# Optimization experiments

Hardware: AMD Instinct MI355X
Metric: run time of the kernel (lower is better)

## Reference

```python
import jax, jax.numpy as jnp
import numpy as np

NQ = 10          # num_qubits
NL = 4           # num_layers (StronglyEntanglingLayers)
DIM = 2 ** NQ    # state-vector dimension = input_linear out features
B = 4096
SEQ = 512
PRED = 96

# ---- static basis-state bookkeeping (wire 0 = most significant bit, as in PennyLane) ----

def _cnot_perm(control, target):
    s = np.arange(DIM)
    bit = (s >> (NQ - 1 - control)) & 1
    return s ^ (bit << (NQ - 1 - target))

def _layer_perms():
    # StronglyEntanglingLayers default ranges: r_l = (l % (n_wires - 1)) + 1,
    # then CNOT(i, (i+r) % n) for i = 0..n-1, applied sequentially.
    perms = []
    for l in range(NL):
        r = (l % (NQ - 1)) + 1
        comp = np.arange(DIM)
        for c in range(NQ):
            g = _cnot_perm(c, (c + r) % NQ)
            comp = comp[g]          # compose: state_new[t] = state_old[comp[t]]
        perms.append(jnp.asarray(comp))
    return perms

PERMS = _layer_perms()

_bits = (np.arange(DIM)[:, None] >> (NQ - 1 - np.arange(NQ))[None, :]) & 1
SIGNS = jnp.asarray(1.0 - 2.0 * _bits, dtype=np.float32)   # [DIM, NQ] PauliZ eigenvalues


def _rot_gates(w):
    # PennyLane Rot(phi, theta, omega) = RZ(omega) @ RY(theta) @ RZ(phi); w: [L, n, 3]
    phi, theta, omega = w[..., 0], w[..., 1], w[..., 2]
    c = jnp.cos(theta / 2)
    s = jnp.sin(theta / 2)
    ep = jnp.exp(0.5j * (phi + omega))   # e^{+i(phi+omega)/2}
    em = jnp.exp(0.5j * (phi - omega))   # e^{+i(phi-omega)/2}
    m00 = jnp.conj(ep) * c
    m01 = -em * s
    m10 = jnp.conj(em) * s
    m11 = ep * c
    return jnp.stack([jnp.stack([m00, m01], -1),
                      jnp.stack([m10, m11], -1)], -2)       # [L, n, 2, 2] complex64


def _apply_1q(psi, U, wire):
    # psi: [B, DIM] complex; apply 2x2 U on `wire`
    b = psi.shape[0]
    left = 2 ** wire
    right = 2 ** (NQ - 1 - wire)
    psi = psi.reshape(b, left, 2, right)
    psi = jnp.einsum('ba,kpaq->kpbq', U, psi)
    return psi.reshape(b, DIM)


def _circuit(psi, q_weights):
    mats = _rot_gates(q_weights)
    for l in range(NL):
        for w in range(NQ):
            psi = _apply_1q(psi, mats[l, w], w)
        psi = psi[:, PERMS[l]]          # composed CNOT ring of this layer
    return psi


def reference(x, W_in, b_in, q_weights, W_out, b_out):
    h = x @ W_in.T + b_in + 1e-6                          # input_linear, then +1e-6
    norm = jnp.linalg.norm(h, axis=-1, keepdims=True)
    psi = (h / norm).astype(jnp.complex64)                # AmplitudeEmbedding(normalize=True)
    psi = _circuit(psi, q_weights)                        # StronglyEntanglingLayers
    probs = psi.real ** 2 + psi.imag ** 2
    expvals = probs @ SIGNS                               # [B, NQ] PauliZ expvals
    return expvals @ W_out.T + b_out                      # output_linear


def setup_inputs() -> dict:
    key = jax.random.key(0)
    ks = jax.random.split(key, 6)
    x = jax.random.normal(ks[0], (B, SEQ), dtype=jnp.float32)
    W_in = jax.random.normal(ks[1], (DIM, SEQ), dtype=jnp.float32) / np.sqrt(SEQ)
    b_in = jax.random.normal(ks[2], (DIM,), dtype=jnp.float32) * 0.01
    q_weights = jax.random.uniform(ks[3], (NL, NQ, 3), dtype=jnp.float32,
                                   minval=0.0, maxval=2.0 * np.pi)
    W_out = jax.random.normal(ks[4], (PRED, NQ), dtype=jnp.float32) / np.sqrt(NQ)
    b_out = jax.random.normal(ks[5], (PRED,), dtype=jnp.float32) * 0.01
    return {"x": x, "W_in": W_in, "b_in": b_in, "q_weights": q_weights,
            "W_out": W_out, "b_out": b_out}
```

## Files before the change

kernel.cpp:

```cpp
#include <hip/hip_runtime.h>
#include <math.h>

#define DIM 1024
#define NQ 10
#define NL 4
#define SEQ 512
#define NROWS 4096
#define PRED 96

typedef unsigned short ushort_t;
typedef unsigned int uint_t;
using half8   = __attribute__((ext_vector_type(8))) _Float16;
using float4v = __attribute__((ext_vector_type(4))) float;

__device__ inline ushort_t f2h(float f) { _Float16 h = (_Float16)f; return *(ushort_t*)&h; }
__device__ inline uint_t pkh(float a, float b) {
    _Float16 ha = (_Float16)a, hb = (_Float16)b;
    return (uint_t)(*(ushort_t*)&ha) | ((uint_t)(*(ushort_t*)&hb) << 16);
}

__global__ __launch_bounds__(256)
void convert_x_kernel(const float* __restrict__ x, ushort_t* __restrict__ xh)
{
    int i = (blockIdx.x * 256 + threadIdx.x) * 8;
    float4 a = *(const float4*)(x + i);
    float4 b = *(const float4*)(x + i + 4);
    uint4 o;
    o.x = pkh(a.x, a.y); o.y = pkh(a.z, a.w);
    o.z = pkh(b.x, b.y); o.w = pkh(b.z, b.w);
    *(uint4*)(xh + i) = o;
}

__global__ __launch_bounds__(512)
void circuit_cols_kernel(const float* __restrict__ Wi, const float* __restrict__ b_in,
                         const float* __restrict__ qw,
                         ushort_t* __restrict__ Crt_r, ushort_t* __restrict__ Crt_i,
                         float* __restrict__ dr, float* __restrict__ di)
{
    __shared__ float2 psi[DIM];
    __shared__ float gm[NL * NQ][8];

    const int tid = threadIdx.x;
    const int j = blockIdx.x;

    if (tid < NL * NQ) {
        float phi = qw[tid * 3 + 0], theta = qw[tid * 3 + 1], omega = qw[tid * 3 + 2];
        float ch = cosf(theta * 0.5f), sh = sinf(theta * 0.5f);
        float a = 0.5f * (phi + omega), b = 0.5f * (phi - omega);
        float ca = cosf(a), sa = sinf(a);
        float cb = cosf(b), sb = sinf(b);
        gm[tid][0] =  ch * ca;  gm[tid][1] = -ch * sa;
        gm[tid][2] = -sh * cb;  gm[tid][3] = -sh * sb;
        gm[tid][4] =  sh * cb;  gm[tid][5] = -sh * sb;
        gm[tid][6] =  ch * ca;  gm[tid][7] =  ch * sa;
    }

    float v0, v1;
    if (j < SEQ) {
        v0 = Wi[(size_t)(2 * tid) * SEQ + j];
        v1 = Wi[(size_t)(2 * tid + 1) * SEQ + j];
    } else {
        v0 = b_in[2 * tid] + 1e-6f;
        v1 = b_in[2 * tid + 1] + 1e-6f;
    }
    psi[2 * tid]     = make_float2(v0, 0.f);
    psi[2 * tid + 1] = make_float2(v1, 0.f);
    __syncthreads();

    for (int l = 0; l < NL; ++l) {
#pragma unroll
        for (int w = 0; w < NQ; ++w) {
            const float* m = gm[l * NQ + w];
            float m00r = m[0], m00i = m[1], m01r = m[2], m01i = m[3];
            float m10r = m[4], m10i = m[5], m11r = m[6], m11i = m[7];
            int mask = 1 << (9 - w);
            int lo = tid & (mask - 1);
            int s0 = ((tid ^ lo) << 1) | lo;
            int s1 = s0 | mask;
            float2 a0 = psi[s0], a1 = psi[s1];
            float2 n0, n1;
            n0.x = m00r * a0.x - m00i * a0.y + m01r * a1.x - m01i * a1.y;
            n0.y = m00r * a0.y + m00i * a0.x + m01r * a1.y + m01i * a1.x;
            n1.x = m10r * a0.x - m10i * a0.y + m11r * a1.x - m11i * a1.y;
            n1.y = m10r * a0.y + m10i * a0.x + m11r * a1.y + m11i * a1.x;
            psi[s0] = n0; psi[s1] = n1;
            __syncthreads();
        }
        int r = l % (NQ - 1) + 1;
        int p0 = tid, p1 = tid + 512;
#pragma unroll
        for (int c = 9; c >= 0; --c) {
            int t = (c + r) % NQ;
            p0 ^= ((p0 >> (9 - c)) & 1) << (9 - t);
            p1 ^= ((p1 >> (9 - c)) & 1) << (9 - t);
        }
        float2 t0 = psi[p0], t1 = psi[p1];
        __syncthreads();
        psi[tid] = t0; psi[tid + 512] = t1;
        __syncthreads();
    }

    float2 o0 = psi[tid], o1 = psi[tid + 512];
    if (j < SEQ) {
        Crt_r[(size_t)tid * SEQ + j]         = f2h(o0.x);
        Crt_i[(size_t)tid * SEQ + j]         = f2h(o0.y);
        Crt_r[(size_t)(tid + 512) * SEQ + j] = f2h(o1.x);
        Crt_i[(size_t)(tid + 512) * SEQ + j] = f2h(o1.y);
    } else {
        dr[tid] = o0.x;        di[tid] = o0.y;
        dr[tid + 512] = o1.x;  di[tid + 512] = o1.y;
    }
}

#define GBM 128
#define GBNC 64
#define GBK 32
#define LDA 40
#define LDP 65

__global__ __launch_bounds__(256)
void gemm_fused_kernel(const ushort_t* __restrict__ xh,
                       const ushort_t* __restrict__ Crt_r, const ushort_t* __restrict__ Crt_i,
                       const float* __restrict__ dr, const float* __restrict__ di,
                       float* __restrict__ part)
{
    __shared__ __align__(16) char lds[GBM * LDP * 4];
    ushort_t* Ash = (ushort_t*)lds;
    ushort_t* Bsr = Ash + GBM * LDA;
    ushort_t* Bsi = Bsr + GBNC * LDA;
    float*    Ps  = (float*)lds;
    __shared__ float drs[GBNC], dis[GBNC];

    const int tid = threadIdx.x;
    const int bm = blockIdx.x, bn = blockIdx.y;
    const int lane = tid & 63, wv = tid >> 6;
    const int n0 = bn * GBNC;

    if (tid < GBNC) { drs[tid] = dr[n0 + tid]; dis[tid] = di[n0 + tid]; }

    float4v accr[2][4], acci[2][4];
#pragma unroll
    for (int a = 0; a < 2; ++a)
#pragma unroll
        for (int b = 0; b < 4; ++b) { accr[a][b] = (float4v)0.f; acci[a][b] = (float4v)0.f; }

    const int sr = tid >> 1, ko = (tid & 1) * 16;
    const ushort_t* xa = xh + (size_t)(bm * GBM + sr) * SEQ + ko;
    const int bsel = tid >> 7;
    const int nr = (tid & 127) >> 1;
    const int bko = (tid & 1) * 16;
    const ushort_t* bsrc = (bsel ? Crt_i : Crt_r) + (size_t)(n0 + nr) * SEQ + bko;
    ushort_t* bdst = (bsel ? Bsi : Bsr) + nr * LDA + bko;

    const int fm = lane & 15, kq = (lane >> 4) * 8;
    const int wrow = wv * 32;

    for (int k0 = 0; k0 < SEQ; k0 += GBK) {
        uint4 a0 = *(const uint4*)(xa + k0);
        uint4 a1 = *(const uint4*)(xa + k0 + 8);
        *(uint4*)(Ash + sr * LDA + ko)     = a0;
        *(uint4*)(Ash + sr * LDA + ko + 8) = a1;
        uint4 b0 = *(const uint4*)(bsrc + k0);
        uint4 b1 = *(const uint4*)(bsrc + k0 + 8);
        *(uint4*)bdst       = b0;
        *(uint4*)(bdst + 8) = b1;
        __syncthreads();

        half8 ah0 = *(half8*)(Ash + (wrow + fm) * LDA + kq);
        half8 ah1 = *(half8*)(Ash + (wrow + 16 + fm) * LDA + kq);
#pragma unroll
        for (int nt = 0; nt < 4; ++nt) {
            half8 br = *(half8*)(Bsr + (nt * 16 + fm) * LDA + kq);
            half8 bi = *(half8*)(Bsi + (nt * 16 + fm) * LDA + kq);
            accr[0][nt] = __builtin_amdgcn_mfma_f32_16x16x32_f16(ah0, br, accr[0][nt], 0, 0, 0);
            accr[1][nt] = __builtin_amdgcn_mfma_f32_16x16x32_f16(ah1, br, accr[1][nt], 0, 0, 0);
            acci[0][nt] = __builtin_amdgcn_mfma_f32_16x16x32_f16(ah0, bi, acci[0][nt], 0, 0, 0);
            acci[1][nt] = __builtin_amdgcn_mfma_f32_16x16x32_f16(ah1, bi, acci[1][nt], 0, 0, 0);
        }
        __syncthreads();
    }

    const int rq = (lane >> 4) * 4;
#pragma unroll
    for (int mt = 0; mt < 2; ++mt)
#pragma unroll
        for (int nt = 0; nt < 4; ++nt) {
            float drv = drs[nt * 16 + fm], div = dis[nt * 16 + fm];
#pragma unroll
            for (int reg = 0; reg < 4; ++reg) {
                int lrow = wrow + mt * 16 + rq + reg;
                float zr = accr[mt][nt][reg] + drv;
                float zi = acci[mt][nt][reg] + div;
                Ps[lrow * LDP + nt * 16 + fm] = zr * zr + zi * zi;
            }
        }
    __syncthreads();

    {
        const int row = tid >> 1, hh = tid & 1;
        const float* pr = Ps + row * LDP + hh * 32;
        float nrm = 0.f, e0 = 0.f, e1 = 0.f, e2 = 0.f, e3 = 0.f, e4 = 0.f, e5 = 0.f;
#pragma unroll
        for (int i = 0; i < 32; ++i) {
            float p = pr[i];
            int c = hh * 32 + i;
            nrm += p;
            e0 += ((c >> 5) & 1) ? -p : p;
            e1 += ((c >> 4) & 1) ? -p : p;
            e2 += ((c >> 3) & 1) ? -p : p;
            e3 += ((c >> 2) & 1) ? -p : p;
            e4 += ((c >> 1) & 1) ? -p : p;
            e5 += (c & 1) ? -p : p;
        }
        size_t base = ((size_t)(bm * GBM + row) * 32 + (bn * 2 + hh)) * 8;
        part[base + 0] = nrm;
        part[base + 1] = e0; part[base + 2] = e1; part[base + 3] = e2;
        part[base + 4] = e3; part[base + 5] = e4; part[base + 6] = e5;
    }
}

__global__ __launch_bounds__(128)
void finalize_kernel(const float* __restrict__ part, const float* __restrict__ W_out,
                     const float* __restrict__ b_out, float* __restrict__ out)
{
    __shared__ float evf[16];
    const int row = blockIdx.x, tid = threadIdx.x;

    if (tid < 64) {
        float v[11];
        if (tid < 32) {
            const float* p = part + ((size_t)row * 32 + tid) * 8;
            float4 a = *(const float4*)p;
            float4 b = *(const float4*)(p + 4);
            float nrm = a.x;
            int bnn = tid >> 1;
            v[0] = nrm;
            v[1] = (bnn & 8) ? -nrm : nrm;
            v[2] = (bnn & 4) ? -nrm : nrm;
            v[3] = (bnn & 2) ? -nrm : nrm;
            v[4] = (bnn & 1) ? -nrm : nrm;
            v[5] = a.y; v[6] = a.z; v[7] = a.w;
            v[8] = b.x; v[9] = b.y; v[10] = b.z;
        } else {
#pragma unroll
            for (int k = 0; k < 11; ++k) v[k] = 0.f;
        }
#pragma unroll
        for (int m = 16; m; m >>= 1)
#pragma unroll
            for (int k = 0; k < 11; ++k) v[k] += __shfl_xor(v[k], m, 64);
        if (tid == 0) {
            float inv = 1.0f / v[0];
#pragma unroll
            for (int k = 0; k < 10; ++k) evf[k] = v[k + 1] * inv;
        }
    }
    __syncthreads();
    if (tid < PRED) {
        float o = b_out[tid];
#pragma unroll
        for (int k = 0; k < NQ; ++k) o = fmaf(W_out[tid * NQ + k], evf[k], o);
        out[(size_t)row * PRED + tid] = o;
    }
}

extern "C" void kernel_launch(void* const* d_in, const int* in_sizes, int n_in,
                              void* d_out, int out_size, void* d_ws, size_t ws_size,
                              hipStream_t stream) {
    const float* x     = (const float*)d_in[0];
    const float* W_in  = (const float*)d_in[1];
    const float* b_in  = (const float*)d_in[2];
    const float* qw    = (const float*)d_in[3];
    const float* W_out = (const float*)d_in[4];
    const float* b_out = (const float*)d_in[5];
    float* out = (float*)d_out;

    char* w = (char*)d_ws;
    const size_t MB = 1u << 20;
    ushort_t* xh    = (ushort_t*)w;
    ushort_t* Crt_r = (ushort_t*)(w + 4 * MB);
    ushort_t* Crt_i = (ushort_t*)(w + 5 * MB);
    float*    dr    = (float*)(w + 6 * MB);
    float*    di    = dr + DIM;
    float*    part  = (float*)(w + 7 * MB);

    convert_x_kernel<<<NROWS * SEQ / (256 * 8), 256, 0, stream>>>(x, xh);
    circuit_cols_kernel<<<SEQ + 1, 512, 0, stream>>>(W_in, b_in, qw, Crt_r, Crt_i, dr, di);
    dim3 g2(NROWS / GBM, DIM / GBNC);
    gemm_fused_kernel<<<g2, 256, 0, stream>>>(xh, Crt_r, Crt_i, dr, di, part);
    finalize_kernel<<<NROWS, 128, 0, stream>>>(part, W_out, b_out, out);
}
```

Baseline: 114.2 us.

## Run circuit per wave in registers with shuffles; fuse x fp16 conversion into GEMM

The circuit kernel now simulates one column per wavefront, not one per 512-thread block. Each lane holds 16 amplitudes in registers: the high qubits use cross-lane shuffles, the low qubits use in-register butterflies, and the CNOT permutation goes through a per-wave LDS scratch with a precomputed permutation table. This removes the many block-wide barriers of the shared-memory version. Separately, the fp32-to-fp16 conversion of x is folded into the GEMM's A-tile load, which drops one launch and the xh round trip but makes the GEMM read twice as many bytes for A. The per-wave scheme leaves fewer blocks (65) on the GPU, and ordering within the wave relies on explicit lgkmcnt waits instead of barriers.

```diff
diff --git a/kernel.cpp b/kernel.cpp
--- a/kernel.cpp
+++ b/kernel.cpp
@@ -19,29 +19,19 @@
     return (uint_t)(*(ushort_t*)&ha) | ((uint_t)(*(ushort_t*)&hb) << 16);
 }
 
-__global__ __launch_bounds__(256)
-void convert_x_kernel(const float* __restrict__ x, ushort_t* __restrict__ xh)
+#define CIRC_WAVES 8
+
+__global__ __launch_bounds__(512)
+void circuit_reg_kernel(const float* __restrict__ Wi, const float* __restrict__ b_in,
+                        const float* __restrict__ qw,
+                        ushort_t* __restrict__ Crt_r, ushort_t* __restrict__ Crt_i,
+                        float* __restrict__ dr, float* __restrict__ di)
 {
-    int i = (blockIdx.x * 256 + threadIdx.x) * 8;
-    float4 a = *(const float4*)(x + i);
-    float4 b = *(const float4*)(x + i + 4);
-    uint4 o;
-    o.x = pkh(a.x, a.y); o.y = pkh(a.z, a.w);
-    o.z = pkh(b.x, b.y); o.w = pkh(b.z, b.w);
-    *(uint4*)(xh + i) = o;
-}
-
-__global__ __launch_bounds__(512)
-void circuit_cols_kernel(const float* __restrict__ Wi, const float* __restrict__ b_in,
-                         const float* __restrict__ qw,
-                         ushort_t* __restrict__ Crt_r, ushort_t* __restrict__ Crt_i,
-                         float* __restrict__ dr, float* __restrict__ di)
-{
-    __shared__ float2 psi[DIM];
     __shared__ float gm[NL * NQ][8];
+    __shared__ ushort_t permtab[NL][DIM];
+    __shared__ float ps[CIRC_WAVES][DIM];
 
     const int tid = threadIdx.x;
-    const int j = blockIdx.x;
 
     if (tid < NL * NQ) {
         float phi = qw[tid * 3 + 0], theta = qw[tid * 3 + 1], omega = qw[tid * 3 + 2];
@@ -55,37 +45,7 @@
         gm[tid][6] =  ch * ca;  gm[tid][7] =  ch * sa;
     }
 
-    float v0, v1;
-    if (j < SEQ) {
-        v0 = Wi[(size_t)(2 * tid) * SEQ + j];
-        v1 = Wi[(size_t)(2 * tid + 1) * SEQ + j];
-    } else {
-        v0 = b_in[2 * tid] + 1e-6f;
-        v1 = b_in[2 * tid + 1] + 1e-6f;
-    }
-    psi[2 * tid]     = make_float2(v0, 0.f);
-    psi[2 * tid + 1] = make_float2(v1, 0.f);
-    __syncthreads();
-
     for (int l = 0; l < NL; ++l) {
-#pragma unroll
-        for (int w = 0; w < NQ; ++w) {
-            const float* m = gm[l * NQ + w];
-            float m00r = m[0], m00i = m[1], m01r = m[2], m01i = m[3];
-            float m10r = m[4], m10i = m[5], m11r = m[6], m11i = m[7];
-            int mask = 1 << (9 - w);
-            int lo = tid & (mask - 1);
-            int s0 = ((tid ^ lo) << 1) | lo;
-            int s1 = s0 | mask;
-            float2 a0 = psi[s0], a1 = psi[s1];
-            float2 n0, n1;
-            n0.x = m00r * a0.x - m00i * a0.y + m01r * a1.x - m01i * a1.y;
-            n0.y = m00r * a0.y + m00i * a0.x + m01r * a1.y + m01i * a1.x;
-            n1.x = m10r * a0.x - m10i * a0.y + m11r * a1.x - m11i * a1.y;
-            n1.y = m10r * a0.y + m10i * a0.x + m11r * a1.y + m11i * a1.x;
-            psi[s0] = n0; psi[s1] = n1;
-            __syncthreads();
-        }
         int r = l % (NQ - 1) + 1;
         int p0 = tid, p1 = tid + 512;
 #pragma unroll
@@ -94,21 +54,96 @@
             p0 ^= ((p0 >> (9 - c)) & 1) << (9 - t);
             p1 ^= ((p1 >> (9 - c)) & 1) << (9 - t);
         }
-        float2 t0 = psi[p0], t1 = psi[p1];
-        __syncthreads();
-        psi[tid] = t0; psi[tid + 512] = t1;
-        __syncthreads();
-    }
-
-    float2 o0 = psi[tid], o1 = psi[tid + 512];
+        permtab[l][tid]       = (ushort_t)p0;
+        permtab[l][tid + 512] = (ushort_t)p1;
+    }
+    __syncthreads();
+
+    const int lane = tid & 63, wv = tid >> 6;
+    const int j = blockIdx.x * CIRC_WAVES + wv;
+    if (j > SEQ) return;
+
+    const int sbase = lane * 16;
+    float2 st[16];
     if (j < SEQ) {
-        Crt_r[(size_t)tid * SEQ + j]         = f2h(o0.x);
-        Crt_i[(size_t)tid * SEQ + j]         = f2h(o0.y);
-        Crt_r[(size_t)(tid + 512) * SEQ + j] = f2h(o1.x);
-        Crt_i[(size_t)(tid + 512) * SEQ + j] = f2h(o1.y);
+#pragma unroll
+        for (int r2 = 0; r2 < 16; ++r2)
+            st[r2] = make_float2(Wi[(size_t)(sbase + r2) * SEQ + j], 0.f);
     } else {
-        dr[tid] = o0.x;        di[tid] = o0.y;
-        dr[tid + 512] = o1.x;  di[tid + 512] = o1.y;
+#pragma unroll
+        for (int r2 = 0; r2 < 16; ++r2)
+            st[r2] = make_float2(b_in[sbase + r2] + 1e-6f, 0.f);
+    }
+
+    float* Pw = ps[wv];
+
+    for (int l = 0; l < NL; ++l) {
+#pragma unroll
+        for (int w = 0; w < 6; ++w) {
+            const float* m = gm[l * NQ + w];
+            const int lb = 5 - w;
+            const int hi = (lane >> lb) & 1;
+            float cAr = hi ? m[6] : m[0];
+            float cAi = hi ? m[7] : m[1];
+            float cBr = hi ? m[4] : m[2];
+            float cBi = hi ? m[5] : m[3];
+            const int mask = 1 << lb;
+#pragma unroll
+            for (int r2 = 0; r2 < 16; ++r2) {
+                float pr = __shfl_xor(st[r2].x, mask, 64);
+                float pi = __shfl_xor(st[r2].y, mask, 64);
+                float nr = cAr * st[r2].x - cAi * st[r2].y + cBr * pr - cBi * pi;
+                float ni = cAr * st[r2].y + cAi * st[r2].x + cBr * pi + cBi * pr;
+                st[r2] = make_float2(nr, ni);
+            }
+        }
+#pragma unroll
+        for (int w = 6; w < 10; ++w) {
+            const float* m = gm[l * NQ + w];
+            float m00r = m[0], m00i = m[1], m01r = m[2], m01i = m[3];
+            float m10r = m[4], m10i = m[5], m11r = m[6], m11i = m[7];
+            const int db = 1 << (9 - w);
+#pragma unroll
+            for (int r0 = 0; r0 < 16; ++r0) {
+                if (r0 & db) continue;
+                const int r1 = r0 | db;
+                float2 a0 = st[r0], a1 = st[r1];
+                st[r0].x = m00r * a0.x - m00i * a0.y + m01r * a1.x - m01i * a1.y;
+                st[r0].y = m00r * a0.y + m00i * a0.x + m01r * a1.y + m01i * a1.x;
+                st[r1].x = m10r * a0.x - m10i * a0.y + m11r * a1.x - m11i * a1.y;
+                st[r1].y = m10r * a0.y + m10i * a0.x + m11r * a1.y + m11i * a1.x;
+            }
+        }
+        const ushort_t* pt = permtab[l];
+        float tmpr[16];
+#pragma unroll
+        for (int r2 = 0; r2 < 16; ++r2) Pw[sbase + r2] = st[r2].x;
+        asm volatile("s_waitcnt lgkmcnt(0)" ::: "memory");
+#pragma unroll
+        for (int r2 = 0; r2 < 16; ++r2) tmpr[r2] = Pw[pt[sbase + r2]];
+        asm volatile("s_waitcnt lgkmcnt(0)" ::: "memory");
+#pragma unroll
+        for (int r2 = 0; r2 < 16; ++r2) Pw[sbase + r2] = st[r2].y;
+        asm volatile("s_waitcnt lgkmcnt(0)" ::: "memory");
+#pragma unroll
+        for (int r2 = 0; r2 < 16; ++r2) {
+            float iy = Pw[pt[sbase + r2]];
+            st[r2] = make_float2(tmpr[r2], iy);
+        }
+    }
+
+    if (j < SEQ) {
+#pragma unroll
+        for (int r2 = 0; r2 < 16; ++r2) {
+            Crt_r[(size_t)(sbase + r2) * SEQ + j] = f2h(st[r2].x);
+            Crt_i[(size_t)(sbase + r2) * SEQ + j] = f2h(st[r2].y);
+        }
+    } else {
+#pragma unroll
+        for (int r2 = 0; r2 < 16; ++r2) {
+            dr[sbase + r2] = st[r2].x;
+            di[sbase + r2] = st[r2].y;
+        }
     }
 }
 
@@ -119,7 +154,7 @@
 #define LDP 65
 
 __global__ __launch_bounds__(256)
-void gemm_fused_kernel(const ushort_t* __restrict__ xh,
+void gemm_fused_kernel(const float* __restrict__ x,
                        const ushort_t* __restrict__ Crt_r, const ushort_t* __restrict__ Crt_i,
                        const float* __restrict__ dr, const float* __restrict__ di,
                        float* __restrict__ part)
@@ -145,7 +180,7 @@
         for (int b = 0; b < 4; ++b) { accr[a][b] = (float4v)0.f; acci[a][b] = (float4v)0.f; }
 
     const int sr = tid >> 1, ko = (tid & 1) * 16;
-    const ushort_t* xa = xh + (size_t)(bm * GBM + sr) * SEQ + ko;
+    const float* xa = x + (size_t)(bm * GBM + sr) * SEQ + ko;
     const int bsel = tid >> 7;
     const int nr = (tid & 127) >> 1;
     const int bko = (tid & 1) * 16;
@@ -156,8 +191,15 @@
     const int wrow = wv * 32;
 
     for (int k0 = 0; k0 < SEQ; k0 += GBK) {
-        uint4 a0 = *(const uint4*)(xa + k0);
-        uint4 a1 = *(const uint4*)(xa + k0 + 8);
+        float4 f0 = *(const float4*)(xa + k0);
+        float4 f1 = *(const float4*)(xa + k0 + 4);
+        float4 f2 = *(const float4*)(xa + k0 + 8);
+        float4 f3 = *(const float4*)(xa + k0 + 12);
+        uint4 a0, a1;
+        a0.x = pkh(f0.x, f0.y); a0.y = pkh(f0.z, f0.w);
+        a0.z = pkh(f1.x, f1.y); a0.w = pkh(f1.z, f1.w);
+        a1.x = pkh(f2.x, f2.y); a1.y = pkh(f2.z, f2.w);
+        a1.z = pkh(f3.x, f3.y); a1.w = pkh(f3.z, f3.w);
         *(uint4*)(Ash + sr * LDA + ko)     = a0;
         *(uint4*)(Ash + sr * LDA + ko + 8) = a1;
         uint4 b0 = *(const uint4*)(bsrc + k0);
@@ -277,16 +319,15 @@
 
     char* w = (char*)d_ws;
     const size_t MB = 1u << 20;
-    ushort_t* xh    = (ushort_t*)w;
-    ushort_t* Crt_r = (ushort_t*)(w + 4 * MB);
-    ushort_t* Crt_i = (ushort_t*)(w + 5 * MB);
-    float*    dr    = (float*)(w + 6 * MB);
+    ushort_t* Crt_r = (ushort_t*)w;
+    ushort_t* Crt_i = (ushort_t*)(w + 1 * MB);
+    float*    dr    = (float*)(w + 2 * MB);
     float*    di    = dr + DIM;
-    float*    part  = (float*)(w + 7 * MB);
-
-    convert_x_kernel<<<NROWS * SEQ / (256 * 8), 256, 0, stream>>>(x, xh);
-    circuit_cols_kernel<<<SEQ + 1, 512, 0, stream>>>(W_in, b_in, qw, Crt_r, Crt_i, dr, di);
+    float*    part  = (float*)(w + 3 * MB);
+
+    circuit_reg_kernel<<<(SEQ + 1 + CIRC_WAVES - 1) / CIRC_WAVES, 512, 0, stream>>>(
+        W_in, b_in, qw, Crt_r, Crt_i, dr, di);
     dim3 g2(NROWS / GBM, DIM / GBNC);
-    gemm_fused_kernel<<<g2, 256, 0, stream>>>(xh, Crt_r, Crt_i, dr, di, part);
+    gemm_fused_kernel<<<g2, 256, 0, stream>>>(x, Crt_r, Crt_i, dr, di, part);
     finalize_kernel<<<NROWS, 128, 0, stream>>>(part, W_out, b_out, out);
 }
```

Result: slower. 137.5 us (+20.4%).

## Restructure circuit kernel to keep amplitudes in registers with wave shuffles

Applied to the files above, without the earlier changes.

Rewrites the per-column circuit simulation so that each of 256 threads holds four amplitudes in registers. Gates on low wires are applied in-thread or through cross-lane shuffles, and only the two highest wires and the CNOT permutation go through double-buffered shared memory. This removes most of the per-gate __syncthreads and shared-memory round trips of the previous version. The cost is more complex index bookkeeping. The circuit kernel is only one of four launches, so its effect on total time is limited.

```diff
diff --git a/kernel.cpp b/kernel.cpp
--- a/kernel.cpp
+++ b/kernel.cpp
@@ -31,14 +31,15 @@
     *(uint4*)(xh + i) = o;
 }
 
-__global__ __launch_bounds__(512)
-void circuit_cols_kernel(const float* __restrict__ Wi, const float* __restrict__ b_in,
-                         const float* __restrict__ qw,
-                         ushort_t* __restrict__ Crt_r, ushort_t* __restrict__ Crt_i,
-                         float* __restrict__ dr, float* __restrict__ di)
+__global__ __launch_bounds__(256)
+void circuit_hybrid_kernel(const float* __restrict__ Wi, const float* __restrict__ b_in,
+                           const float* __restrict__ qw,
+                           ushort_t* __restrict__ Crt_r, ushort_t* __restrict__ Crt_i,
+                           float* __restrict__ dr, float* __restrict__ di)
 {
-    __shared__ float2 psi[DIM];
     __shared__ float gm[NL * NQ][8];
+    __shared__ float bre[2][DIM];
+    __shared__ float bim[2][DIM];
 
     const int tid = threadIdx.x;
     const int j = blockIdx.x;
@@ -55,60 +56,169 @@
         gm[tid][6] =  ch * ca;  gm[tid][7] =  ch * sa;
     }
 
-    float v0, v1;
+    float2 st[4];
     if (j < SEQ) {
-        v0 = Wi[(size_t)(2 * tid) * SEQ + j];
-        v1 = Wi[(size_t)(2 * tid + 1) * SEQ + j];
+#pragma unroll
+        for (int r = 0; r < 4; ++r)
+            st[r] = make_float2(Wi[(size_t)(tid * 4 + r) * SEQ + j], 0.f);
     } else {
-        v0 = b_in[2 * tid] + 1e-6f;
-        v1 = b_in[2 * tid + 1] + 1e-6f;
-    }
-    psi[2 * tid]     = make_float2(v0, 0.f);
-    psi[2 * tid + 1] = make_float2(v1, 0.f);
+#pragma unroll
+        for (int r = 0; r < 4; ++r)
+            st[r] = make_float2(b_in[tid * 4 + r] + 1e-6f, 0.f);
+    }
+#pragma unroll
+    for (int r = 0; r < 4; ++r) {
+        bre[0][r * 256 + tid] = st[r].x;
+        bim[0][r * 256 + tid] = st[r].y;
+    }
     __syncthreads();
-
+    int cur = 0;
+
+    {
+        const float* m = gm[0];
+        const int hi = tid >> 7;
+        float cAr = hi ? m[6] : m[0], cAi = hi ? m[7] : m[1];
+        float cBr = hi ? m[4] : m[2], cBi = hi ? m[5] : m[3];
+#pragma unroll
+        for (int r = 0; r < 4; ++r) {
+            float px = bre[cur][r * 256 + (tid ^ 128)];
+            float py = bim[cur][r * 256 + (tid ^ 128)];
+            float nx = cAr * st[r].x - cAi * st[r].y + cBr * px - cBi * py;
+            float ny = cAr * st[r].y + cAi * st[r].x + cBr * py + cBi * px;
+            st[r] = make_float2(nx, ny);
+        }
+    }
+
+#pragma unroll
     for (int l = 0; l < NL; ++l) {
-#pragma unroll
-        for (int w = 0; w < NQ; ++w) {
+        {
+#pragma unroll
+            for (int r = 0; r < 4; ++r) {
+                bre[cur ^ 1][r * 256 + tid] = st[r].x;
+                bim[cur ^ 1][r * 256 + tid] = st[r].y;
+            }
+            __syncthreads();
+            cur ^= 1;
+            const float* m = gm[l * NQ + 1];
+            const int hi = (tid >> 6) & 1;
+            float cAr = hi ? m[6] : m[0], cAi = hi ? m[7] : m[1];
+            float cBr = hi ? m[4] : m[2], cBi = hi ? m[5] : m[3];
+#pragma unroll
+            for (int r = 0; r < 4; ++r) {
+                float px = bre[cur][r * 256 + (tid ^ 64)];
+                float py = bim[cur][r * 256 + (tid ^ 64)];
+                float nx = cAr * st[r].x - cAi * st[r].y + cBr * px - cBi * py;
+                float ny = cAr * st[r].y + cAi * st[r].x + cBr * py + cBi * px;
+                st[r] = make_float2(nx, ny);
+            }
+        }
+#pragma unroll
+        for (int w = 2; w < 8; ++w) {
             const float* m = gm[l * NQ + w];
+            const int lb = 7 - w;
+            const int hi = (tid >> lb) & 1;
+            float cAr = hi ? m[6] : m[0], cAi = hi ? m[7] : m[1];
+            float cBr = hi ? m[4] : m[2], cBi = hi ? m[5] : m[3];
+            const int mask = 1 << lb;
+#pragma unroll
+            for (int r = 0; r < 4; ++r) {
+                float px = __shfl_xor(st[r].x, mask, 64);
+                float py = __shfl_xor(st[r].y, mask, 64);
+                float nx = cAr * st[r].x - cAi * st[r].y + cBr * px - cBi * py;
+                float ny = cAr * st[r].y + cAi * st[r].x + cBr * py + cBi * px;
+                st[r] = make_float2(nx, ny);
+            }
+        }
+        {
+            const float* m = gm[l * NQ + 8];
             float m00r = m[0], m00i = m[1], m01r = m[2], m01i = m[3];
             float m10r = m[4], m10i = m[5], m11r = m[6], m11i = m[7];
-            int mask = 1 << (9 - w);
-            int lo = tid & (mask - 1);
-            int s0 = ((tid ^ lo) << 1) | lo;
-            int s1 = s0 | mask;
-            float2 a0 = psi[s0], a1 = psi[s1];
-            float2 n0, n1;
-            n0.x = m00r * a0.x - m00i * a0.y + m01r * a1.x - m01i * a1.y;
-            n0.y = m00r * a0.y + m00i * a0.x + m01r * a1.y + m01i * a1.x;
-            n1.x = m10r * a0.x - m10i * a0.y + m11r * a1.x - m11i * a1.y;
-            n1.y = m10r * a0.y + m10i * a0.x + m11r * a1.y + m11i * a1.x;
-            psi[s0] = n0; psi[s1] = n1;
+#pragma unroll
+            for (int r0 = 0; r0 < 2; ++r0) {
+                float2 a0 = st[r0], a1 = st[r0 + 2];
+                st[r0].x     = m00r * a0.x - m00i * a0.y + m01r * a1.x - m01i * a1.y;
+                st[r0].y     = m00r * a0.y + m00i * a0.x + m01r * a1.y + m01i * a1.x;
+                st[r0 + 2].x = m10r * a0.x - m10i * a0.y + m11r * a1.x - m11i * a1.y;
+                st[r0 + 2].y = m10r * a0.y + m10i * a0.x + m11r * a1.y + m11i * a1.x;
+            }
+        }
+        {
+            const float* m = gm[l * NQ + 9];
+            float m00r = m[0], m00i = m[1], m01r = m[2], m01i = m[3];
+            float m10r = m[4], m10i = m[5], m11r = m[6], m11i = m[7];
+#pragma unroll
+            for (int r0 = 0; r0 < 4; r0 += 2) {
+                float2 a0 = st[r0], a1 = st[r0 + 1];
+                st[r0].x     = m00r * a0.x - m00i * a0.y + m01r * a1.x - m01i * a1.y;
+                st[r0].y     = m00r * a0.y + m00i * a0.x + m01r * a1.y + m01i * a1.x;
+                st[r0 + 1].x = m10r * a0.x - m10i * a0.y + m11r * a1.x - m11i * a1.y;
+                st[r0 + 1].y = m10r * a0.y + m10i * a0.x + m11r * a1.y + m11i * a1.x;
+            }
+        }
+        {
+#pragma unroll
+            for (int r = 0; r < 4; ++r) {
+                bre[cur ^ 1][r * 256 + tid] = st[r].x;
+                bim[cur ^ 1][r * 256 + tid] = st[r].y;
+            }
             __syncthreads();
-        }
-        int r = l % (NQ - 1) + 1;
-        int p0 = tid, p1 = tid + 512;
-#pragma unroll
-        for (int c = 9; c >= 0; --c) {
-            int t = (c + r) % NQ;
-            p0 ^= ((p0 >> (9 - c)) & 1) << (9 - t);
-            p1 ^= ((p1 >> (9 - c)) & 1) << (9 - t);
-        }
-        float2 t0 = psi[p0], t1 = psi[p1];
-        __syncthreads();
-        psi[tid] = t0; psi[tid + 512] = t1;
-        __syncthreads();
-    }
-
-    float2 o0 = psi[tid], o1 = psi[tid + 512];
+            cur ^= 1;
+
+            const int rr = l % (NQ - 1) + 1;
+            int pbase = tid * 4;
+            int p1 = 1, p2 = 2, p512 = 512;
+#pragma unroll
+            for (int c = 9; c >= 0; --c) {
+                const int t = (c + rr) % NQ;
+                pbase ^= ((pbase >> (9 - c)) & 1) << (9 - t);
+                p1    ^= ((p1    >> (9 - c)) & 1) << (9 - t);
+                p2    ^= ((p2    >> (9 - c)) & 1) << (9 - t);
+                p512  ^= ((p512  >> (9 - c)) & 1) << (9 - t);
+            }
+            const int p3 = p1 ^ p2;
+            const int prr0 = pbase, prr1 = pbase ^ p1, prr2 = pbase ^ p2, prr3 = pbase ^ p3;
+            int Ps[4] = {prr0, prr1, prr2, prr3};
+
+            if (l < NL - 1) {
+                const float* m = gm[(l + 1) * NQ + 0];
+                const int hi = tid >> 7;
+                float cAr = hi ? m[6] : m[0], cAi = hi ? m[7] : m[1];
+                float cBr = hi ? m[4] : m[2], cBi = hi ? m[5] : m[3];
+#pragma unroll
+                for (int r = 0; r < 4; ++r) {
+                    int so = Ps[r];
+                    int sp = so ^ p512;
+                    int io = (so >> 2) | ((so & 3) << 8);
+                    int ip = (sp >> 2) | ((sp & 3) << 8);
+                    float ox = bre[cur][io], oy = bim[cur][io];
+                    float px = bre[cur][ip], py = bim[cur][ip];
+                    float nx = cAr * ox - cAi * oy + cBr * px - cBi * py;
+                    float ny = cAr * oy + cAi * ox + cBr * py + cBi * px;
+                    st[r] = make_float2(nx, ny);
+                }
+            } else {
+#pragma unroll
+                for (int r = 0; r < 4; ++r) {
+                    int so = Ps[r];
+                    int io = (so >> 2) | ((so & 3) << 8);
+                    st[r] = make_float2(bre[cur][io], bim[cur][io]);
+                }
+            }
+        }
+    }
+
     if (j < SEQ) {
-        Crt_r[(size_t)tid * SEQ + j]         = f2h(o0.x);
-        Crt_i[(size_t)tid * SEQ + j]         = f2h(o0.y);
-        Crt_r[(size_t)(tid + 512) * SEQ + j] = f2h(o1.x);
-        Crt_i[(size_t)(tid + 512) * SEQ + j] = f2h(o1.y);
+#pragma unroll
+        for (int r = 0; r < 4; ++r) {
+            Crt_r[(size_t)(tid * 4 + r) * SEQ + j] = f2h(st[r].x);
+            Crt_i[(size_t)(tid * 4 + r) * SEQ + j] = f2h(st[r].y);
+        }
     } else {
-        dr[tid] = o0.x;        di[tid] = o0.y;
-        dr[tid + 512] = o1.x;  di[tid + 512] = o1.y;
+#pragma unroll
+        for (int r = 0; r < 4; ++r) {
+            dr[tid * 4 + r] = st[r].x;
+            di[tid * 4 + r] = st[r].y;
+        }
     }
 }
 
@@ -285,7 +395,7 @@
     float*    part  = (float*)(w + 7 * MB);
 
     convert_x_kernel<<<NROWS * SEQ / (256 * 8), 256, 0, stream>>>(x, xh);
-    circuit_cols_kernel<<<SEQ + 1, 512, 0, stream>>>(W_in, b_in, qw, Crt_r, Crt_i, dr, di);
+    circuit_hybrid_kernel<<<SEQ + 1, 256, 0, stream>>>(W_in, b_in, qw, Crt_r, Crt_i, dr, di);
     dim3 g2(NROWS / GBM, DIM / GBNC);
     gemm_fused_kernel<<<g2, 256, 0, stream>>>(xh, Crt_r, Crt_i, dr, di, part);
     finalize_kernel<<<NROWS, 128, 0, stream>>>(part, W_out, b_out, out);
```

Result: faster. 111.6 us (-2.2%).
